# Kernel tuning notes

Hardware: AMD Instinct MI355X
Metric: run time of the kernel (lower is better)

The kernel has to match this reference:

```python
import jax, jax.numpy as jnp
import numpy as np

B, C, N, M, K = 1, 64, 65536, 65536, 16
H, O = 64, 128  # mlp hidden, out_channels


def setup_inputs() -> dict:
    key = jax.random.key(0)
    ks = jax.random.split(key, 8)
    return {
        "x": jax.random.normal(ks[0], (B, C, N), dtype=jnp.float32),
        "pos": jax.random.normal(ks[1], (B, 3, N), dtype=jnp.float32),
        "support_points": jax.random.normal(ks[2], (B, 3, M), dtype=jnp.float32),
        "W1": jax.random.normal(ks[3], (H, C + 3), dtype=jnp.float32) * 0.05,
        "b1": jax.random.normal(ks[4], (H,), dtype=jnp.float32) * 0.05,
        "W2": jax.random.normal(ks[5], (O, H), dtype=jnp.float32) * 0.05,
        "b2": jax.random.normal(ks[6], (O,), dtype=jnp.float32) * 0.05,
        "indices": jax.random.randint(ks[7], (B, M, K), 0, N, dtype=jnp.int64),
    }


def _gather_points(t, indices):
    # t: [B, C, N], indices: [B, M, K] -> [B, C, M, K]
    b, c, n = t.shape
    m, k = indices.shape[1], indices.shape[2]
    idx = indices.reshape(b, 1, m * k)  # broadcasts over channel dim
    return jnp.take_along_axis(t, idx, axis=2).reshape(b, c, m, k)


def reference(x, pos, support_points, W1, b1, W2, b2, indices):
    # gather neighbor features and positions: [B, C, M, K], [B, 3, M, K]
    feats = _gather_points(x, indices)
    pts = _gather_points(pos, indices) - support_points[:, :, :, None]
    h = jnp.concatenate([feats, pts], axis=1)  # [B, C+3, M, K]
    # shared per-point MLP (1x1 Conv2d == channel contraction)
    h = jnp.einsum("oc,bcmk->bomk", W1, h) + b1[None, :, None, None]
    h = jax.nn.relu(h)
    h = jnp.einsum("oc,bcmk->bomk", W2, h) + b2[None, :, None, None]
    # max-pool over neighborhood K -> [B, O, M]
    return jnp.max(h, axis=3)
```

## Files before the change

kernel.cpp:

```cpp
#include <hip/hip_runtime.h>

#define NPTS 65536
#define MPTS 65536

typedef __attribute__((ext_vector_type(8))) short bf16x8;
typedef __attribute__((ext_vector_type(4))) float f32x4;

__device__ __forceinline__ float bflo(unsigned int u){ union{unsigned int i; float f;} v; v.i = u<<16; return v.f; }
__device__ __forceinline__ float bfhi(unsigned int u){ union{unsigned int i; float f;} v; v.i = u & 0xffff0000u; return v.f; }
__device__ __forceinline__ unsigned short f2bf(float f){
  union{float f; unsigned int i;} v; v.f=f;
  unsigned int r = v.i + 0x7fffu + ((v.i>>16)&1u);
  return (unsigned short)(r>>16);
}

__global__ __launch_bounds__(256) void pack_points(
    const float* __restrict__ x, const float* __restrict__ pos,
    unsigned short* __restrict__ P2) {
  __shared__ unsigned short tile[256 * 72];
  const int t = threadIdx.x;
  const int n0 = blockIdx.x * 256;
  #pragma unroll 8
  for (int c = 0; c < 64; ++c) tile[t*72 + c] = f2bf(x[(size_t)c * NPTS + n0 + t]);
  #pragma unroll
  for (int d = 0; d < 3; ++d) tile[t*72 + 64 + d] = f2bf(pos[(size_t)d * NPTS + n0 + t]);
  #pragma unroll
  for (int c = 67; c < 72; ++c) tile[t*72 + c] = 0;
  __syncthreads();
  const unsigned int* tD = (const unsigned int*)tile;
  unsigned int* pD = (unsigned int*)P2 + (size_t)n0 * 36;
  #pragma unroll 4
  for (int i = 0; i < 36; ++i) pD[t + i*256] = tD[t + i*256];
}

__global__ __launch_bounds__(256) void pack_wf(
    const float* __restrict__ W1, const float* __restrict__ W2,
    unsigned short* __restrict__ W1F, unsigned short* __restrict__ W2F) {
  const int f = blockIdx.x * 256 + threadIdx.x;
  if (f < 768) {
    const int kt = f >> 8, rem = f & 255, nt = rem >> 6, lane = rem & 63;
    const int h = nt*16 + (lane & 15);
    const int c0 = kt*32 + (lane >> 4) * 8;
    #pragma unroll
    for (int j = 0; j < 8; ++j) {
      const int c = c0 + j;
      W1F[f*8 + j] = (c < 67) ? f2bf(W1[h*67 + c]) : (unsigned short)0;
    }
  } else if (f < 1792) {
    const int g = f - 768;
    const int kt = g >> 9, rem = g & 511, ot = rem >> 6, lane = rem & 63;
    const int o = ot*16 + (lane & 15);
    const int h0 = kt*32 + (lane >> 4) * 8;
    #pragma unroll
    for (int j = 0; j < 8; ++j) W2F[g*8 + j] = f2bf(W2[o*64 + h0 + j]);
  }
}

#define MFMA16(a,b,c) __builtin_amdgcn_mfma_f32_16x16x32_bf16((a),(b),(c),0,0,0)

__global__ __launch_bounds__(256, 2) void pointnet_mfma(
    const unsigned short* __restrict__ P2,
    const float* __restrict__ sup,
    const unsigned short* __restrict__ W1F,
    const float* __restrict__ b1,
    const unsigned short* __restrict__ W2F,
    const float* __restrict__ b2,
    const int* __restrict__ indices,
    float* __restrict__ out) {
  __shared__ __align__(16) char smem[53248];
  unsigned short* featB = (unsigned short*)smem;
  unsigned short* hlds  = (unsigned short*)smem;
  float* smax = (float*)(smem + 40960);

  const int t = threadIdx.x;
  const int m0 = blockIdx.x * 16;
  const int lane = t & 63, w = t >> 6, quad = lane >> 4, lr = lane & 15;

  {
    const int idx = indices[m0*16 + t];
    const uint4* src = (const uint4*)(P2 + (size_t)idx * 72);
    uint4* dst = (uint4*)(featB + t * 104);
    uint4 u[9];
    #pragma unroll
    for (int i = 0; i < 9; ++i) u[i] = src[i];
    const int mm = m0 + (t >> 4);
    const float s0 = sup[mm], s1 = sup[MPTS + mm], s2 = sup[2*MPTS + mm];
    const float p0 = bflo(u[8].x), p1 = bfhi(u[8].x), p2 = bflo(u[8].y);
    u[8].x = (unsigned int)f2bf(p0 - s0) | ((unsigned int)f2bf(p1 - s1) << 16);
    u[8].y = (unsigned int)f2bf(p2 - s2);
    u[8].z = 0u; u[8].w = 0u;
    #pragma unroll
    for (int i = 0; i < 9; ++i) dst[i] = u[i];
    const uint4 z = {0u, 0u, 0u, 0u};
    dst[9] = z; dst[10] = z; dst[11] = z;
  }

  bf16x8 w1f[3][4];
  #pragma unroll
  for (int kt = 0; kt < 3; ++kt)
    #pragma unroll
    for (int nt = 0; nt < 4; ++nt)
      w1f[kt][nt] = ((const bf16x8*)W1F)[(kt*4 + nt)*64 + lane];
  float b1s[4];
  #pragma unroll
  for (int nt = 0; nt < 4; ++nt) b1s[nt] = b1[nt*16 + lr];

  __syncthreads();

  const f32x4 fz = {0.f, 0.f, 0.f, 0.f};
  f32x4 acc[4][4];
  #pragma unroll
  for (int pt = 0; pt < 4; ++pt)
    #pragma unroll
    for (int nt = 0; nt < 4; ++nt) acc[pt][nt] = fz;
  #pragma unroll
  for (int kt = 0; kt < 3; ++kt) {
    bf16x8 af[4];
    #pragma unroll
    for (int pt = 0; pt < 4; ++pt)
      af[pt] = *(const bf16x8*)&featB[(w*64 + pt*16 + lr)*104 + kt*32 + quad*8];
    #pragma unroll
    for (int pt = 0; pt < 4; ++pt)
      #pragma unroll
      for (int nt = 0; nt < 4; ++nt)
        acc[pt][nt] = MFMA16(af[pt], w1f[kt][nt], acc[pt][nt]);
  }

  __syncthreads();

  #pragma unroll
  for (int pt = 0; pt < 4; ++pt)
    #pragma unroll
    for (int nt = 0; nt < 4; ++nt) {
      const int h = nt*16 + lr;
      #pragma unroll
      for (int r = 0; r < 4; ++r) {
        const int p = w*64 + pt*16 + quad*4 + r;
        hlds[p*72 + h] = f2bf(fmaxf(acc[pt][nt][r] + b1s[nt], 0.f));
      }
    }
  __syncthreads();

  #pragma unroll
  for (int oh = 0; oh < 2; ++oh) {
    bf16x8 w2f[2][4];
    #pragma unroll
    for (int kt = 0; kt < 2; ++kt)
      #pragma unroll
      for (int ot = 0; ot < 4; ++ot)
        w2f[kt][ot] = ((const bf16x8*)W2F)[(kt*8 + oh*4 + ot)*64 + lane];
    f32x4 a2[4][4];
    #pragma unroll
    for (int pt = 0; pt < 4; ++pt)
      #pragma unroll
      for (int ot = 0; ot < 4; ++ot) a2[pt][ot] = fz;
    #pragma unroll
    for (int kt = 0; kt < 2; ++kt) {
      bf16x8 ah[4];
      #pragma unroll
      for (int pt = 0; pt < 4; ++pt)
        ah[pt] = *(const bf16x8*)&hlds[(w*64 + pt*16 + lr)*72 + kt*32 + quad*8];
      #pragma unroll
      for (int pt = 0; pt < 4; ++pt)
        #pragma unroll
        for (int ot = 0; ot < 4; ++ot)
          a2[pt][ot] = MFMA16(ah[pt], w2f[kt][ot], a2[pt][ot]);
    }
    #pragma unroll
    for (int pt = 0; pt < 4; ++pt)
      #pragma unroll
      for (int ot = 0; ot < 4; ++ot) {
        f32x4 v4 = a2[pt][ot];
        float v = fmaxf(fmaxf(v4[0], v4[1]), fmaxf(v4[2], v4[3]));
        v = fmaxf(v, __shfl_xor(v, 16));
        v = fmaxf(v, __shfl_xor(v, 32));
        if (quad == 0) smax[(w*4 + pt)*128 + oh*64 + ot*16 + lr] = v;
      }
  }
  __syncthreads();

  #pragma unroll
  for (int i = 0; i < 2; ++i) {
    const int u = t + i*256;
    const int o = u >> 2, mg = u & 3;
    const float bb = b2[o];
    float4 val;
    val.x = smax[(mg*4 + 0)*128 + o] + bb;
    val.y = smax[(mg*4 + 1)*128 + o] + bb;
    val.z = smax[(mg*4 + 2)*128 + o] + bb;
    val.w = smax[(mg*4 + 3)*128 + o] + bb;
    *(float4*)(out + (size_t)o * MPTS + m0 + mg*4) = val;
  }
}

__global__ __launch_bounds__(256) void pointnet_fallback(
    const float* __restrict__ x, const float* __restrict__ pos,
    const float* __restrict__ sup,
    const float* __restrict__ W1, const float* __restrict__ b1,
    const float* __restrict__ W2, const float* __restrict__ b2,
    const int* __restrict__ indices, float* __restrict__ out) {
  __shared__ float sfeat[16][68];
  __shared__ float shid[16][64];
  __shared__ float smax[4][128];
  __shared__ int sidx[16];
  const int t = threadIdx.x;
  const int m = blockIdx.x;
  if (t < 16) sidx[t] = indices[m*16 + t];
  const float sup0 = sup[m], sup1 = sup[MPTS + m], sup2 = sup[2*MPTS + m];
  __syncthreads();
  for (int u = t; u < 16*17; u += 256) {
    const int k = u / 17, c4 = (u - k*17) * 4;
    const int idx = sidx[k];
    float4 w;
    if (c4 < 64) {
      w.x = x[(size_t)(c4+0)*NPTS + idx]; w.y = x[(size_t)(c4+1)*NPTS + idx];
      w.z = x[(size_t)(c4+2)*NPTS + idx]; w.w = x[(size_t)(c4+3)*NPTS + idx];
    } else {
      w.x = pos[idx] - sup0; w.y = pos[NPTS + idx] - sup1;
      w.z = pos[2*NPTS + idx] - sup2; w.w = 0.f;
    }
    *(float4*)&sfeat[k][c4] = w;
  }
  const int h = t & 63, kg = t >> 6;
  float w1r[68];
  #pragma unroll
  for (int c = 0; c < 67; ++c) w1r[c] = W1[h*67 + c];
  w1r[67] = 0.f;
  const float bias1 = b1[h];
  __syncthreads();
  #pragma unroll
  for (int j = 0; j < 4; ++j) {
    const int k = kg*4 + j;
    float a = bias1;
    const float4* rr = (const float4*)sfeat[k];
    #pragma unroll
    for (int q = 0; q < 17; ++q) {
      const float4 v = rr[q];
      a += w1r[q*4+0]*v.x + w1r[q*4+1]*v.y + w1r[q*4+2]*v.z + w1r[q*4+3]*v.w;
    }
    shid[k][h] = fmaxf(a, 0.f);
  }
  const int ow = t & 63;
  float w2a[64], w2b[64];
  #pragma unroll
  for (int hh = 0; hh < 64; ++hh) { w2a[hh] = W2[ow*64 + hh]; w2b[hh] = W2[(ow+64)*64 + hh]; }
  __syncthreads();
  float mxa = -3.0e38f, mxb = -3.0e38f;
  #pragma unroll
  for (int j = 0; j < 4; ++j) {
    const int k = kg*4 + j;
    const float4* hr = (const float4*)shid[k];
    float pa = 0.f, pb = 0.f;
    #pragma unroll
    for (int q = 0; q < 16; ++q) {
      const float4 v = hr[q];
      pa += w2a[q*4+0]*v.x + w2a[q*4+1]*v.y + w2a[q*4+2]*v.z + w2a[q*4+3]*v.w;
      pb += w2b[q*4+0]*v.x + w2b[q*4+1]*v.y + w2b[q*4+2]*v.z + w2b[q*4+3]*v.w;
    }
    mxa = fmaxf(mxa, pa); mxb = fmaxf(mxb, pb);
  }
  smax[kg][ow] = mxa; smax[kg][64 + ow] = mxb;
  __syncthreads();
  if (t < 128) {
    out[(size_t)t * MPTS + m] =
        fmaxf(fmaxf(smax[0][t], smax[1][t]), fmaxf(smax[2][t], smax[3][t])) + b2[t];
  }
}

extern "C" void kernel_launch(void* const* d_in, const int* in_sizes, int n_in,
                              void* d_out, int out_size, void* d_ws, size_t ws_size,
                              hipStream_t stream) {
  const float* x   = (const float*)d_in[0];
  const float* pos = (const float*)d_in[1];
  const float* sup = (const float*)d_in[2];
  const float* W1  = (const float*)d_in[3];
  const float* b1  = (const float*)d_in[4];
  const float* W2  = (const float*)d_in[5];
  const float* b2  = (const float*)d_in[6];
  const int* indices = (const int*)d_in[7];
  float* out = (float*)d_out;

  const size_t P2_BYTES  = (size_t)NPTS * 72 * 2;
  const size_t W1F_BYTES = 768 * 8 * 2;
  const size_t W2F_BYTES = 1024 * 8 * 2;
  if (ws_size >= P2_BYTES + W1F_BYTES + W2F_BYTES) {
    unsigned short* P2  = (unsigned short*)d_ws;
    unsigned short* W1F = (unsigned short*)((char*)d_ws + P2_BYTES);
    unsigned short* W2F = (unsigned short*)((char*)d_ws + P2_BYTES + W1F_BYTES);
    pack_points<<<NPTS/256, 256, 0, stream>>>(x, pos, P2);
    pack_wf<<<7, 256, 0, stream>>>(W1, W2, W1F, W2F);
    pointnet_mfma<<<MPTS/16, 256, 0, stream>>>(P2, sup, W1F, b1, W2F, b2, indices, out);
  } else {
    pointnet_fallback<<<MPTS, 256, 0, stream>>>(x, pos, sup, W1, b1, W2, b2, indices, out);
  }
}
```

Before: 151.5 us.

## Fuse pack kernels, shrink LDS stride, drop block barriers, raise occupancy

Merges the point and weight packing kernels into one launch and repacks points with a 64-point tile and a padded LDS layout. In the main kernel, the LDS row stride drops from 104 to 88. The zero-padding stores are removed; the third K tile instead masks the lanes that would read past the valid channels. Block-wide barriers are dropped because each wave only touches its own rows, and launch bounds are raised to 3 blocks per CU. The aim is less LDS traffic, less synchronisation and higher occupancy, at the cost of tighter register and LDS budgets.

```diff
diff --git a/kernel.cpp b/kernel.cpp
--- a/kernel.cpp
+++ b/kernel.cpp
@@ -2,6 +2,7 @@
 
 #define NPTS 65536
 #define MPTS 65536
+#define FSTR 88
 
 typedef __attribute__((ext_vector_type(8))) short bf16x8;
 typedef __attribute__((ext_vector_type(4))) float f32x4;
@@ -14,51 +15,65 @@
   return (unsigned short)(r>>16);
 }
 
-__global__ __launch_bounds__(256) void pack_points(
+__global__ __launch_bounds__(256) void pack_all(
     const float* __restrict__ x, const float* __restrict__ pos,
-    unsigned short* __restrict__ P2) {
-  __shared__ unsigned short tile[256 * 72];
+    const float* __restrict__ W1, const float* __restrict__ W2,
+    unsigned short* __restrict__ P2,
+    unsigned short* __restrict__ W1F, unsigned short* __restrict__ W2F) {
+  __shared__ unsigned int tile[64 * 37];
   const int t = threadIdx.x;
-  const int n0 = blockIdx.x * 256;
-  #pragma unroll 8
-  for (int c = 0; c < 64; ++c) tile[t*72 + c] = f2bf(x[(size_t)c * NPTS + n0 + t]);
-  #pragma unroll
-  for (int d = 0; d < 3; ++d) tile[t*72 + 64 + d] = f2bf(pos[(size_t)d * NPTS + n0 + t]);
-  #pragma unroll
-  for (int c = 67; c < 72; ++c) tile[t*72 + c] = 0;
-  __syncthreads();
-  const unsigned int* tD = (const unsigned int*)tile;
-  unsigned int* pD = (unsigned int*)P2 + (size_t)n0 * 36;
-  #pragma unroll 4
-  for (int i = 0; i < 36; ++i) pD[t + i*256] = tD[t + i*256];
-}
-
-__global__ __launch_bounds__(256) void pack_wf(
-    const float* __restrict__ W1, const float* __restrict__ W2,
-    unsigned short* __restrict__ W1F, unsigned short* __restrict__ W2F) {
-  const int f = blockIdx.x * 256 + threadIdx.x;
-  if (f < 768) {
-    const int kt = f >> 8, rem = f & 255, nt = rem >> 6, lane = rem & 63;
-    const int h = nt*16 + (lane & 15);
-    const int c0 = kt*32 + (lane >> 4) * 8;
-    #pragma unroll
-    for (int j = 0; j < 8; ++j) {
-      const int c = c0 + j;
-      W1F[f*8 + j] = (c < 67) ? f2bf(W1[h*67 + c]) : (unsigned short)0;
-    }
-  } else if (f < 1792) {
-    const int g = f - 768;
-    const int kt = g >> 9, rem = g & 511, ot = rem >> 6, lane = rem & 63;
-    const int o = ot*16 + (lane & 15);
-    const int h0 = kt*32 + (lane >> 4) * 8;
-    #pragma unroll
-    for (int j = 0; j < 8; ++j) W2F[g*8 + j] = f2bf(W2[o*64 + h0 + j]);
+  const int n0 = blockIdx.x * 64;
+  const int p = t & 63, cq = t >> 6;
+  const int n = n0 + p;
+  #pragma unroll
+  for (int jj = 0; jj < 8; ++jj) {
+    const int c = cq * 16 + 2 * jj;
+    const unsigned int lo = f2bf(x[(size_t)c * NPTS + n]);
+    const unsigned int hi = f2bf(x[(size_t)(c + 1) * NPTS + n]);
+    tile[p * 37 + cq * 8 + jj] = lo | (hi << 16);
+  }
+  if (cq == 0) {
+    const unsigned int a = f2bf(pos[n]);
+    const unsigned int b = f2bf(pos[NPTS + n]);
+    const unsigned int cc = f2bf(pos[2 * NPTS + n]);
+    tile[p * 37 + 32] = a | (b << 16);
+    tile[p * 37 + 33] = cc;
+    tile[p * 37 + 34] = 0u;
+    tile[p * 37 + 35] = 0u;
+  }
+  __syncthreads();
+  unsigned int* Pd = (unsigned int*)(P2 + (size_t)n0 * 72);
+  #pragma unroll
+  for (int i = 0; i < 9; ++i) {
+    const int u = t + i * 256;
+    const int nl = u / 36, d = u - nl * 36;
+    Pd[u] = tile[nl * 37 + d];
+  }
+  if (blockIdx.x < 7) {
+    const int f = blockIdx.x * 256 + t;
+    if (f < 768) {
+      const int kt = f >> 8, rem = f & 255, nt = rem >> 6, lane = rem & 63;
+      const int h = nt*16 + (lane & 15);
+      const int c0 = kt*32 + (lane >> 4) * 8;
+      #pragma unroll
+      for (int j = 0; j < 8; ++j) {
+        const int c = c0 + j;
+        W1F[f*8 + j] = (c < 67) ? f2bf(W1[h*67 + c]) : (unsigned short)0;
+      }
+    } else if (f < 1792) {
+      const int g = f - 768;
+      const int kt = g >> 9, rem = g & 511, ot = rem >> 6, lane = rem & 63;
+      const int o = ot*16 + (lane & 15);
+      const int h0 = kt*32 + (lane >> 4) * 8;
+      #pragma unroll
+      for (int j = 0; j < 8; ++j) W2F[g*8 + j] = f2bf(W2[o*64 + h0 + j]);
+    }
   }
 }
 
 #define MFMA16(a,b,c) __builtin_amdgcn_mfma_f32_16x16x32_bf16((a),(b),(c),0,0,0)
 
-__global__ __launch_bounds__(256, 2) void pointnet_mfma(
+__global__ __launch_bounds__(256, 3) void pointnet_mfma(
     const unsigned short* __restrict__ P2,
     const float* __restrict__ sup,
     const unsigned short* __restrict__ W1F,
@@ -70,7 +85,7 @@
   __shared__ __align__(16) char smem[53248];
   unsigned short* featB = (unsigned short*)smem;
   unsigned short* hlds  = (unsigned short*)smem;
-  float* smax = (float*)(smem + 40960);
+  float* smax = (float*)(smem + 45056);
 
   const int t = threadIdx.x;
   const int m0 = blockIdx.x * 16;
@@ -79,7 +94,6 @@
   {
     const int idx = indices[m0*16 + t];
     const uint4* src = (const uint4*)(P2 + (size_t)idx * 72);
-    uint4* dst = (uint4*)(featB + t * 104);
     uint4 u[9];
     #pragma unroll
     for (int i = 0; i < 9; ++i) u[i] = src[i];
@@ -89,10 +103,9 @@
     u[8].x = (unsigned int)f2bf(p0 - s0) | ((unsigned int)f2bf(p1 - s1) << 16);
     u[8].y = (unsigned int)f2bf(p2 - s2);
     u[8].z = 0u; u[8].w = 0u;
+    uint4* dst = (uint4*)(featB + t * FSTR);
     #pragma unroll
     for (int i = 0; i < 9; ++i) dst[i] = u[i];
-    const uint4 z = {0u, 0u, 0u, 0u};
-    dst[9] = z; dst[10] = z; dst[11] = z;
   }
 
   bf16x8 w1f[3][4];
@@ -105,8 +118,6 @@
   #pragma unroll
   for (int nt = 0; nt < 4; ++nt) b1s[nt] = b1[nt*16 + lr];
 
-  __syncthreads();
-
   const f32x4 fz = {0.f, 0.f, 0.f, 0.f};
   f32x4 acc[4][4];
   #pragma unroll
@@ -114,32 +125,42 @@
     #pragma unroll
     for (int nt = 0; nt < 4; ++nt) acc[pt][nt] = fz;
   #pragma unroll
-  for (int kt = 0; kt < 3; ++kt) {
+  for (int kt = 0; kt < 2; ++kt) {
     bf16x8 af[4];
     #pragma unroll
     for (int pt = 0; pt < 4; ++pt)
-      af[pt] = *(const bf16x8*)&featB[(w*64 + pt*16 + lr)*104 + kt*32 + quad*8];
+      af[pt] = *(const bf16x8*)&featB[(w*64 + pt*16 + lr)*FSTR + kt*32 + quad*8];
     #pragma unroll
     for (int pt = 0; pt < 4; ++pt)
       #pragma unroll
       for (int nt = 0; nt < 4; ++nt)
         acc[pt][nt] = MFMA16(af[pt], w1f[kt][nt], acc[pt][nt]);
   }
-
-  __syncthreads();
+  {
+    const bf16x8 zv = {0,0,0,0,0,0,0,0};
+    bf16x8 af[4];
+    #pragma unroll
+    for (int pt = 0; pt < 4; ++pt) {
+      const bf16x8 v = *(const bf16x8*)&featB[(w*64 + pt*16 + lr)*FSTR + 64];
+      af[pt] = (quad == 0) ? v : zv;
+    }
+    #pragma unroll
+    for (int pt = 0; pt < 4; ++pt)
+      #pragma unroll
+      for (int nt = 0; nt < 4; ++nt)
+        acc[pt][nt] = MFMA16(af[pt], w1f[2][nt], acc[pt][nt]);
+  }
 
   #pragma unroll
   for (int pt = 0; pt < 4; ++pt)
     #pragma unroll
     for (int nt = 0; nt < 4; ++nt) {
       const int h = nt*16 + lr;
-      #pragma unroll
-      for (int r = 0; r < 4; ++r) {
-        const int p = w*64 + pt*16 + quad*4 + r;
-        hlds[p*72 + h] = f2bf(fmaxf(acc[pt][nt][r] + b1s[nt], 0.f));
-      }
-    }
-  __syncthreads();
+      const int pbase = w*64 + pt*16 + quad*4;
+      #pragma unroll
+      for (int r = 0; r < 4; ++r)
+        hlds[(pbase + r)*FSTR + h] = f2bf(fmaxf(acc[pt][nt][r] + b1s[nt], 0.f));
+    }
 
   #pragma unroll
   for (int oh = 0; oh < 2; ++oh) {
@@ -159,7 +180,7 @@
       bf16x8 ah[4];
       #pragma unroll
       for (int pt = 0; pt < 4; ++pt)
-        ah[pt] = *(const bf16x8*)&hlds[(w*64 + pt*16 + lr)*72 + kt*32 + quad*8];
+        ah[pt] = *(const bf16x8*)&hlds[(w*64 + pt*16 + lr)*FSTR + kt*32 + quad*8];
       #pragma unroll
       for (int pt = 0; pt < 4; ++pt)
         #pragma unroll
@@ -287,8 +308,7 @@
     unsigned short* P2  = (unsigned short*)d_ws;
     unsigned short* W1F = (unsigned short*)((char*)d_ws + P2_BYTES);
     unsigned short* W2F = (unsigned short*)((char*)d_ws + P2_BYTES + W1F_BYTES);
-    pack_points<<<NPTS/256, 256, 0, stream>>>(x, pos, P2);
-    pack_wf<<<7, 256, 0, stream>>>(W1, W2, W1F, W2F);
+    pack_all<<<NPTS/64, 256, 0, stream>>>(x, pos, W1, W2, P2, W1F, W2F);
     pointnet_mfma<<<MPTS/16, 256, 0, stream>>>(P2, sup, W1F, b1, W2F, b2, indices, out);
   } else {
     pointnet_fallback<<<MPTS, 256, 0, stream>>>(x, pos, sup, W1, b1, W2, b2, indices, out);
```

New measurement: 153.3 us. No clear change (+1.2%).
